# Optimization experiments

Hardware: AMD Instinct MI355X
Metric: run time of the kernel (lower is better)

Reference implementation:

```python
import jax, jax.numpy as jnp
import numpy as np
import math

B, S, HID = 1, 2048, 2048
H, QLR, KVLR = 16, 1536, 512
NOPE, ROPE, VD = 128, 64, 128
QKD = NOPE + ROPE


def rmsnorm(x, w, eps=1e-6):
    v = jnp.mean(x * x, axis=-1, keepdims=True)
    return w * (x * jax.lax.rsqrt(v + eps))


def rope_tables(seq_len, dim):
    inv_freq = 1.0 / (10000.0 ** (jnp.arange(0, dim, 2, dtype=jnp.float32) / dim))
    t = jnp.arange(seq_len, dtype=jnp.float32)[:, None]
    freqs = t * inv_freq[None, :]
    freqs = jnp.concatenate([freqs, freqs], axis=-1)  # [S, dim]
    return jnp.cos(freqs), jnp.sin(freqs)


def rotate_half(x):
    x1, x2 = jnp.split(x, 2, axis=-1)
    return jnp.concatenate([-x2, x1], axis=-1)


def setup_inputs() -> dict:
    key = jax.random.key(0)
    ks = jax.random.split(key, 8)
    s = 0.02
    return {
        'x': jax.random.normal(ks[0], (B, S, HID), jnp.float32),
        'wq_a_w': jax.random.normal(ks[1], (QLR, HID), jnp.float32) * s,
        'wq_a_b': jnp.zeros((QLR,), jnp.float32),
        'q_norm_w': jnp.ones((QLR,), jnp.float32),
        'wq_b_w': jax.random.normal(ks[2], (H * QKD, QLR), jnp.float32) * s,
        'wq_b_b': jnp.zeros((H * QKD,), jnp.float32),
        'wkv_a_w': jax.random.normal(ks[3], (KVLR + ROPE, HID), jnp.float32) * s,
        'wkv_a_b': jnp.zeros((KVLR + ROPE,), jnp.float32),
        'kv_norm_w': jnp.ones((KVLR,), jnp.float32),
        'wkv_b_w': jax.random.normal(ks[4], (H * (NOPE + VD), KVLR), jnp.float32) * s,
        'wo_w': jax.random.normal(ks[5], (HID, H * VD), jnp.float32) * s,
        'wo_b': jnp.zeros((HID,), jnp.float32),
    }


def reference(x, wq_a_w, wq_a_b, q_norm_w, wq_b_w, wq_b_b, wkv_a_w, wkv_a_b,
              kv_norm_w, wkv_b_w, wo_w, wo_b):
    bs, seq_len, _ = x.shape
    # low-rank q projection
    q = x @ wq_a_w.T + wq_a_b            # [B,S,QLR]
    q = rmsnorm(q, q_norm_w)
    q = q @ wq_b_w.T + wq_b_b            # [B,S,H*QKD]
    q = q.reshape(bs, seq_len, H, QKD)
    q_nope, q_pe = q[..., :NOPE], q[..., NOPE:]

    # latent kv + rope key
    kv_full = x @ wkv_a_w.T + wkv_a_b    # [B,S,KVLR+ROPE]
    kv, k_pe = kv_full[..., :KVLR], kv_full[..., KVLR:]

    cos, sin = rope_tables(seq_len, ROPE)        # [S,ROPE]
    cos4 = cos[None, :, None, :]
    sin4 = sin[None, :, None, :]
    q_pe = q_pe * cos4 + rotate_half(q_pe) * sin4          # [B,S,H,ROPE]
    k_pe = k_pe * cos[None] + rotate_half(k_pe) * sin[None]  # [B,S,ROPE]

    # absorbed kv projection
    wkv_b = wkv_b_w.reshape(H, NOPE + VD, KVLR)
    q_nope = jnp.einsum('bshd,hdc->bshc', q_nope, wkv_b[:, :NOPE])  # [B,S,H,KVLR]
    kv = rmsnorm(kv, kv_norm_w)                                     # [B,T,KVLR]

    scores = (jnp.einsum('bshc,btc->bsht', q_nope, kv)
              + jnp.einsum('bshr,btr->bsht', q_pe, k_pe)) / math.sqrt(QKD)
    # causal mask: position t > s masked
    s_idx = jnp.arange(seq_len)
    mask = jnp.where(s_idx[None, :, None, None] >= s_idx[None, None, None, :],
                     0.0, -jnp.inf)  # [1,S,1,T]
    scores = jax.nn.softmax(scores + mask, axis=-1)

    out = jnp.einsum('bsht,btc->bshc', scores, kv)            # [B,S,H,KVLR]
    out = jnp.einsum('bshc,hdc->bshd', out, wkv_b[:, NOPE:])  # [B,S,H,VD]
    out = out.reshape(bs, seq_len, H * VD)
    return out @ wo_w.T + wo_b
```

## Files before the change

### kernel.cpp

```cpp
#include <hip/hip_runtime.h>
#include <hip/hip_bf16.h>
#include <stdint.h>


using bf16 = __hip_bfloat16;
typedef __bf16 bf16x8 __attribute__((ext_vector_type(8)));
typedef __bf16 bf16x4 __attribute__((ext_vector_type(4)));
typedef float f32x4 __attribute__((ext_vector_type(4)));

#define S_LEN 2048
#define NHEAD 16

static __device__ __forceinline__ void gload16(const void* g, void* l) {
  __builtin_amdgcn_global_load_lds(
      (const __attribute__((address_space(1))) unsigned int*)g,
      (__attribute__((address_space(3))) unsigned int*)l, 16, 0, 0);
}

__global__ void cvt_all(const float* __restrict__ x, const float* __restrict__ wqa_s,
                        const float* __restrict__ wqb_s, const float* __restrict__ wkva_s,
                        const float* __restrict__ wkvb_s, const float* __restrict__ wo_s,
                        bf16* __restrict__ xb, bf16* __restrict__ wqa,
                        bf16* __restrict__ wqb, bf16* __restrict__ wkva,
                        bf16* __restrict__ wkvb, bf16* __restrict__ wob) {
  const size_t n0 = 1048576;
  const size_t n1 = n0 + 786432;
  const size_t n2 = n1 + 1179648;
  const size_t n3 = n2 + 327680;
  const size_t n4 = n3 + 524288;
  const size_t n5 = n4 + 1048576;
  auto cvt4 = [](const float4 v, bf16* d) {
    bf16x4 o;
    o[0] = (__bf16)__float2bfloat16(v.x);
    o[1] = (__bf16)__float2bfloat16(v.y);
    o[2] = (__bf16)__float2bfloat16(v.z);
    o[3] = (__bf16)__float2bfloat16(v.w);
    *(bf16x4*)d = o;
  };
  for (size_t i = (size_t)blockIdx.x * blockDim.x + threadIdx.x; i < n5;
       i += (size_t)gridDim.x * blockDim.x) {
    if (i < n0) {
      cvt4(*(const float4*)(x + i * 4), xb + i * 4);
    } else if (i < n1) {
      size_t j = i - n0;
      cvt4(*(const float4*)(wqa_s + j * 4), wqa + j * 4);
    } else if (i < n2) {
      size_t j = i - n1;
      cvt4(*(const float4*)(wqb_s + j * 4), wqb + j * 4);
    } else if (i < n3) {
      size_t j = i - n2;
      size_t e = j * 4;
      int r = (int)(e / 2048), c = (int)(e % 2048);
      float4 v = (r < 576) ? *(const float4*)(wkva_s + (size_t)r * 2048 + c)
                           : make_float4(0.f, 0.f, 0.f, 0.f);
      cvt4(v, wkva + e);
    } else if (i < n4) {
      size_t j = i - n3;
      cvt4(*(const float4*)(wkvb_s + j * 4), wkvb + j * 4);
    } else {
      size_t j = i - n4;
      cvt4(*(const float4*)(wo_s + j * 4), wob + j * 4);
    }
  }
}

__global__ void rmsnorm_bf16(const bf16* __restrict__ in, const float* __restrict__ w,
                             bf16* __restrict__ out, int cols) {
  const int r = blockIdx.x, tid = threadIdx.x;
  const bf16* row = in + (size_t)r * cols;
  float ss = 0.f;
  for (int c = tid; c < cols; c += 256) {
    float v = __bfloat162float(row[c]);
    ss += v * v;
  }
  for (int m = 32; m >= 1; m >>= 1) ss += __shfl_xor(ss, m, 64);
  __shared__ float red[4];
  if ((tid & 63) == 0) red[tid >> 6] = ss;
  __syncthreads();
  ss = red[0] + red[1] + red[2] + red[3];
  float inv = rsqrtf(ss / (float)cols + 1e-6f);
  for (int c = tid; c < cols; c += 256)
    out[(size_t)r * cols + c] = __float2bfloat16(__bfloat162float(row[c]) * inv * w[c]);
}

__global__ void kv_post(const float* __restrict__ kvf, const float* __restrict__ kvw,
                        bf16* __restrict__ kvn, bf16* __restrict__ Kh) {
  const int t = blockIdx.x, tid = threadIdx.x;
  const float* row = kvf + (size_t)t * 640;
  float ss = 0.f;
  for (int c = tid; c < 512; c += 256) { float v = row[c]; ss += v * v; }
  for (int m = 32; m >= 1; m >>= 1) ss += __shfl_xor(ss, m, 64);
  __shared__ float red[4];
  if ((tid & 63) == 0) red[tid >> 6] = ss;
  __syncthreads();
  ss = red[0] + red[1] + red[2] + red[3];
  float inv = rsqrtf(ss * (1.0f / 512.0f) + 1e-6f);
  for (int c = tid; c < 512; c += 256)
    kvn[(size_t)t * 512 + c] = __float2bfloat16(row[c] * inv * kvw[c]);
  if (tid < 32) {
    const int j = tid;
    float freq = expf(-(float)j * (1.0f / 32.0f) * 9.210340371976184f);
    float ang = (float)t * freq;
    float cs = cosf(ang), sn = sinf(ang);
    float x1 = row[512 + j];
    float x2 = row[512 + j + 32];
    bf16 o1 = __float2bfloat16(x1 * cs - x2 * sn);
    bf16 o2 = __float2bfloat16(x2 * cs + x1 * sn);
#pragma unroll
    for (int h = 0; h < 16; ++h) {
      bf16* kr = Kh + ((size_t)h * S_LEN + t) * 192 + 128;
      kr[j] = o1;
      kr[j + 32] = o2;
    }
  }
}

__global__ void q_rope(bf16* __restrict__ qv) {
  const int s = blockIdx.x, tid = threadIdx.x;
  for (int it = tid; it < 512; it += 256) {
    const int h = it >> 5, j = it & 31;
    float freq = expf(-(float)j * (1.0f / 32.0f) * 9.210340371976184f);
    float ang = (float)s * freq;
    float cs = cosf(ang), sn = sinf(ang);
    bf16* base = qv + (size_t)s * 3072 + h * 192 + 128;
    float x1 = __bfloat162float(base[j]);
    float x2 = __bfloat162float(base[j + 32]);
    base[j] = __float2bfloat16(x1 * cs - x2 * sn);
    base[j + 32] = __float2bfloat16(x2 * cs + x1 * sn);
  }
}

__global__ __launch_bounds__(256, 3)
void attn_flash(const bf16* __restrict__ qv, const bf16* __restrict__ Kh,
                const bf16* __restrict__ V2T, bf16* __restrict__ oabs) {
  const int lin = (int)blockIdx.x + 32 * (int)blockIdx.y;
  const int l2 = (lin & 7) * 64 + (lin >> 3);
  const int h = l2 >> 5;
  const int qb = 31 - (l2 & 31);
  const int tid = threadIdx.x, w = tid >> 6, lane = tid & 63;
  const int lo = lane & 15, hi = lane >> 4;
  __shared__ bf16 Kn[2][32 * 128];
  __shared__ bf16 Kr[2][32 * 64];
  __shared__ bf16 Vt[2][128 * 32];
  __shared__ bf16 Pl[4][16 * 40];
  const int q0 = qb * 64 + w * 16;
  const int q = q0 + lo;

  bf16x8 Qf[6];
  {
    const bf16* qp = qv + (size_t)(q0 + lo) * 3072 + h * 192 + hi * 8;
#pragma unroll
    for (int ks = 0; ks < 6; ++ks) Qf[ks] = *(const bf16x8*)(qp + ks * 32);
  }
  f32x4 o[8];
#pragma unroll
  for (int cg = 0; cg < 8; ++cg) o[cg] = (f32x4){0.f, 0.f, 0.f, 0.f};
  float mrow = -3e38f, lrow = 0.f;

  const bf16* khh = Kh + (size_t)h * S_LEN * 192;
  const bf16* vth = V2T + (size_t)h * 128 * S_LEN;

  auto stage = [&](int tt, int b) {
    const int t0s = tt * 32;
#pragma unroll
    for (int i = 0; i < 2; ++i) {
      const int c = w * 2 + i;
      const int row = c * 4 + (lane >> 4);
      gload16(khh + (size_t)(t0s + row) * 192 + (((lane & 15) ^ (row & 7)) << 3),
              &Kn[b][c * 512]);
    }
#pragma unroll
    for (int i = 0; i < 2; ++i) {
      const int c = w * 2 + i;
      const int row = c * 16 + (lane >> 2);
      gload16(vth + (size_t)row * S_LEN + t0s + ((lane & 3) << 3),
              &Vt[b][c * 512]);
    }
    {
      const int row = w * 8 + (lane >> 3);
      gload16(khh + (size_t)(t0s + row) * 192 + 128 + ((((lane & 7) ^ (row & 7))) << 3),
              &Kr[b][w * 512]);
    }
  };

  const int ntile = 2 * qb + 2;
  stage(0, 0);
  for (int t = 0; t < ntile; ++t) {
    __syncthreads();
    const int b = t & 1;
    if (t + 1 < ntile) stage(t + 1, b ^ 1);
    const int t0 = t * 32;

    f32x4 sc[2];
    sc[0] = (f32x4){0.f, 0.f, 0.f, 0.f};
    sc[1] = (f32x4){0.f, 0.f, 0.f, 0.f};
#pragma unroll
    for (int ks = 0; ks < 4; ++ks)
#pragma unroll
      for (int f = 0; f < 2; ++f) {
        const int row = f * 16 + lo;
        bf16x8 kf = *(const bf16x8*)&Kn[b][row * 128 + (((ks << 2) + hi) ^ (lo & 7)) * 8];
        sc[f] = __builtin_amdgcn_mfma_f32_16x16x32_bf16(kf, Qf[ks], sc[f], 0, 0, 0);
      }
#pragma unroll
    for (int kk2 = 0; kk2 < 2; ++kk2)
#pragma unroll
      for (int f = 0; f < 2; ++f) {
        const int row = f * 16 + lo;
        bf16x8 kf = *(const bf16x8*)&Kr[b][row * 64 + (((kk2 << 2) + hi) ^ (lo & 7)) * 8];
        sc[f] = __builtin_amdgcn_mfma_f32_16x16x32_bf16(kf, Qf[4 + kk2], sc[f], 0, 0, 0);
      }

    const bool diag = (t0 + 31 > q0);
    float rmax = -3e38f;
#pragma unroll
    for (int f = 0; f < 2; ++f)
#pragma unroll
      for (int j = 0; j < 4; ++j) {
        float v = sc[f][j] * 0.0721687836487032f;
        if (diag && (t0 + f * 16 + hi * 4 + j > q)) v = -3e38f;
        sc[f][j] = v;
        rmax = fmaxf(rmax, v);
      }
    rmax = fmaxf(rmax, __shfl_xor(rmax, 16, 64));
    rmax = fmaxf(rmax, __shfl_xor(rmax, 32, 64));

    const float mn = fmaxf(mrow, rmax);
    const float fsc = __expf(mrow - mn);
    mrow = mn;

    float rsum = 0.f;
    bf16* prow = &Pl[w][lo * 40];
#pragma unroll
    for (int f = 0; f < 2; ++f) {
      float pj[4];
#pragma unroll
      for (int j = 0; j < 4; ++j) {
        pj[j] = __expf(sc[f][j] - mn);
        rsum += pj[j];
      }
#pragma unroll
      for (int i2 = 0; i2 < 2; ++i2) {
        uint32_t lo16 = (uint32_t)__bfloat16_as_ushort(__float2bfloat16(pj[i2 * 2]));
        uint32_t hi16 = (uint32_t)__bfloat16_as_ushort(__float2bfloat16(pj[i2 * 2 + 1]));
        *(uint32_t*)(prow + f * 16 + hi * 4 + i2 * 2) = lo16 | (hi16 << 16);
      }
    }
    rsum += __shfl_xor(rsum, 16, 64);
    rsum += __shfl_xor(rsum, 32, 64);
    lrow = lrow * fsc + rsum;

    float fscO[4];
#pragma unroll
    for (int j = 0; j < 4; ++j) fscO[j] = __shfl(fsc, hi * 4 + j, 64);
#pragma unroll
    for (int cg = 0; cg < 8; ++cg)
#pragma unroll
      for (int j = 0; j < 4; ++j) o[cg][j] *= fscO[j];

    bf16x8 pa = *(const bf16x8*)&Pl[w][lo * 40 + hi * 8];
#pragma unroll
    for (int cg = 0; cg < 8; ++cg) {
      bf16x8 vf = *(const bf16x8*)&Vt[b][(cg * 16 + lo) * 32 + hi * 8];
      o[cg] = __builtin_amdgcn_mfma_f32_16x16x32_bf16(pa, vf, o[cg], 0, 0, 0);
    }
  }

  const float linv = 1.0f / lrow;
  float linvO[4];
#pragma unroll
  for (int j = 0; j < 4; ++j) linvO[j] = __shfl(linv, hi * 4 + j, 64);
  bf16* ob = oabs + (size_t)q0 * 2048 + h * 128;
#pragma unroll
  for (int j = 0; j < 4; ++j)
#pragma unroll
    for (int cg = 0; cg < 8; ++cg)
      ob[(size_t)(hi * 4 + j) * 2048 + cg * 16 + lo] =
          __float2bfloat16(o[cg][j] * linvO[j]);
}

template <bool BIAS, bool BF16OUT, int BM>
__global__ __launch_bounds__(256)
void gemm_bt(const bf16* __restrict__ A, const bf16* __restrict__ B,
             const float* __restrict__ bias, void* __restrict__ Cv,
             int lda, int ldb, int ldc, int K, int Nreal,
             long long bA, long long bB, long long bC, int mode) {
  int bx, byi, bz;
  {
    const int gx = gridDim.x, gy = gridDim.y;
    const int nwg = gx * gy * (int)gridDim.z;
    const int lin = (int)blockIdx.x + gx * ((int)blockIdx.y + gy * (int)blockIdx.z);
    const int cpx = nwg >> 3;
    const int l2 = (lin & 7) * cpx + (lin >> 3);
    bx = l2 % gx;
    byi = (l2 / gx) % gy;
    bz = l2 / (gx * gy);
    if (mode) byi = (bz & 1) ? byi : gy - 1 - byi;
  }
  const size_t m0 = (size_t)byi * BM, n0 = (size_t)bx * 128;
  if (mode == 1 && (int)n0 >= (int)m0 + BM) return;
  const int Keff = (mode == 2) ? ((K < (int)m0 + BM) ? K : (int)m0 + BM) : K;

  constexpr int ACH = BM / 8;
  constexpr int PER = (ACH + 16) / 4;
  constexpr int NFR = (BM == 64) ? 2 : 4;
  __shared__ bf16 As[2][BM * 64];
  __shared__ bf16 Bs[2][8192];
  const int tid = threadIdx.x;
  const int wave = tid >> 6, lane = tid & 63;
  const int lo = lane & 15, hi = lane >> 4;
  const int rowbase = (BM == 64) ? 0 : ((wave >> 1) * 64);
  const int colbase = (BM == 64) ? (wave * 32) : ((wave & 1) * 64);
  A += (size_t)bz * (size_t)bA;
  B += (size_t)bz * (size_t)bB;
  const int srow = lane >> 3;
  const int scol = (((lane & 7) ^ srow) * 8);
  const int rsw = lo & 7;

  auto stage = [&](int k0, int buf) {
#pragma unroll
    for (int i = 0; i < PER; ++i) {
      const int blk = wave * PER + i;
      if (blk < ACH) {
        const int row = blk * 8 + srow;
        gload16(A + (m0 + row) * (size_t)lda + k0 + scol, &As[buf][blk * 512]);
      } else {
        const int j = blk - ACH;
        const int row = j * 8 + srow;
        gload16(B + (n0 + row) * (size_t)ldb + k0 + scol, &Bs[buf][j * 512]);
      }
    }
  };

  f32x4 acc[4][NFR] = {};
  stage(0, 0);
  int cur = 0;
  for (int k0 = 0; k0 < Keff; k0 += 64) {
    __syncthreads();
    if (k0 + 64 < Keff) stage(k0 + 64, cur ^ 1);
#pragma unroll
    for (int kk = 0; kk < 2; ++kk) {
      const int ch = (((kk << 2) + hi) ^ rsw) << 3;
      bf16x8 af[4], bfr[NFR];
#pragma unroll
      for (int m = 0; m < 4; ++m)
        af[m] = *(const bf16x8*)&As[cur][(rowbase + m * 16 + lo) * 64 + ch];
#pragma unroll
      for (int n = 0; n < NFR; ++n)
        bfr[n] = *(const bf16x8*)&Bs[cur][(colbase + n * 16 + lo) * 64 + ch];
#pragma unroll
      for (int m = 0; m < 4; ++m)
#pragma unroll
        for (int n = 0; n < NFR; ++n)
          acc[m][n] = __builtin_amdgcn_mfma_f32_16x16x32_bf16(af[m], bfr[n], acc[m][n], 0, 0, 0);
    }
    cur ^= 1;
  }
  float* Cf = (float*)Cv;
  bf16* Cb = (bf16*)Cv;
  const size_t cbase = (size_t)bz * (size_t)bC;
#pragma unroll
  for (int m = 0; m < 4; ++m) {
    const size_t row = m0 + rowbase + m * 16 + hi * 4;
#pragma unroll
    for (int n = 0; n < NFR; ++n) {
      const int col = (int)n0 + colbase + n * 16 + lo;
      if (col < Nreal) {
        const float bv = BIAS ? bias[col] : 0.0f;
#pragma unroll
        for (int j = 0; j < 4; ++j) {
          const float v = acc[m][n][j] + bv;
          const size_t off = cbase + (row + j) * (size_t)ldc + col;
          if (BF16OUT) Cb[off] = __float2bfloat16(v);
          else         Cf[off] = v;
        }
      }
    }
  }
}

extern "C" void kernel_launch(void* const* d_in, const int* in_sizes, int n_in,
                              void* d_out, int out_size, void* d_ws, size_t ws_size,
                              hipStream_t stream) {
  const float* x       = (const float*)d_in[0];
  const float* wq_a_w  = (const float*)d_in[1];
  const float* wq_a_b  = (const float*)d_in[2];
  const float* q_norm  = (const float*)d_in[3];
  const float* wq_b_w  = (const float*)d_in[4];
  const float* wq_b_b  = (const float*)d_in[5];
  const float* wkv_a_w = (const float*)d_in[6];
  const float* wkv_a_b = (const float*)d_in[7];
  const float* kv_norm = (const float*)d_in[8];
  const float* wkv_b_w = (const float*)d_in[9];
  const float* wo_w    = (const float*)d_in[10];
  const float* wo_bias = (const float*)d_in[11];
  float* out = (float*)d_out;

  char* base = (char*)d_ws;
  bf16*  xb   = (bf16*)(base + 0);
  bf16*  wqa  = (bf16*)(base + 8388608);
  bf16*  wqb  = (bf16*)(base + 14680064);
  bf16*  wkva = (bf16*)(base + 24117248);
  bf16*  wkvb = (bf16*)(base + 26738688);
  bf16*  qa   = (bf16*)(base + 30932992);
  bf16*  qn   = (bf16*)(base + 37224448);
  float* kvf  = (float*)(base + 43515904);
  bf16*  kvn  = (bf16*)(base + 48758784);
  char* q = base + 134217728;
  bf16* qv   = (bf16*)(q);             q += 12582912;
  bf16* Kh   = (bf16*)(q);             q += 12582912;
  bf16* V2T  = (bf16*)(q);             q += 8388608;
  bf16* wob  = (bf16*)(q);             q += 8388608;
  bf16* oabs = (bf16*)(q);             q += 8388608;

  cvt_all<<<dim3(2048), 256, 0, stream>>>(x, wq_a_w, wq_b_w, wkv_a_w, wkv_b_w, wo_w,
                                          xb, wqa, wqb, wkva, wkvb, wob);

  gemm_bt<true, true, 64><<<dim3(12, 32, 1), 256, 0, stream>>>(
      xb, wqa, wq_a_b, qa, 2048, 2048, 1536, 2048, 1536, 0, 0, 0, 0);
  rmsnorm_bf16<<<2048, 256, 0, stream>>>(qa, q_norm, qn, 1536);
  gemm_bt<true, true, 128><<<dim3(24, 16, 1), 256, 0, stream>>>(
      qn, wqb, wq_b_b, qv, 1536, 1536, 3072, 1536, 3072, 0, 0, 0, 0);
  q_rope<<<2048, 256, 0, stream>>>(qv);
  gemm_bt<true, false, 64><<<dim3(5, 32, 1), 256, 0, stream>>>(
      xb, wkva, wkv_a_b, kvf, 2048, 2048, 640, 2048, 576, 0, 0, 0, 0);
  kv_post<<<2048, 256, 0, stream>>>(kvf, kv_norm, kvn, Kh);
  gemm_bt<false, true, 64><<<dim3(1, 32, 16), 256, 0, stream>>>(
      kvn, wkvb, nullptr, Kh, 512, 512, 192, 512, 128,
      0, 256ll * 512, 2048ll * 192, 0);
  gemm_bt<false, true, 64><<<dim3(16, 2, 16), 256, 0, stream>>>(
      wkvb + 128ull * 512, kvn, nullptr, V2T, 512, 512, 2048, 512, 2048,
      256ll * 512, 0, 128ll * 2048, 0);

  attn_flash<<<dim3(32, 16), 256, 0, stream>>>(qv, Kh, V2T, oabs);

  gemm_bt<true, false, 64><<<dim3(16, 32, 1), 256, 0, stream>>>(
      oabs, wob, wo_bias, out, 2048, 2048, 2048, 2048, 2048, 0, 0, 0, 0);
}
```

Before: 258.7 us.

## Use 64-key tiles in flash attention, load rope keys from global, skip rescales

The attention kernel now processes 64 keys per iteration instead of 32, which halves the number of tile iterations and barriers. V tiles get an XOR swizzle, and the rope-key part is loaded straight from global memory into registers instead of being staged in LDS. Rescaling of the output accumulator is skipped when no row's running max changes. The larger LDS footprint and more registers drop the occupancy target from 3 to 2 blocks per SM, and the direct global rope loads may add latency.

```diff
diff --git a/kernel.cpp b/kernel.cpp
--- a/kernel.cpp
+++ b/kernel.cpp
@@ -130,7 +130,7 @@
   }
 }
 
-__global__ __launch_bounds__(256, 3)
+__global__ __launch_bounds__(256, 2)
 void attn_flash(const bf16* __restrict__ qv, const bf16* __restrict__ Kh,
                 const bf16* __restrict__ V2T, bf16* __restrict__ oabs) {
   const int lin = (int)blockIdx.x + 32 * (int)blockIdx.y;
@@ -139,10 +139,9 @@
   const int qb = 31 - (l2 & 31);
   const int tid = threadIdx.x, w = tid >> 6, lane = tid & 63;
   const int lo = lane & 15, hi = lane >> 4;
-  __shared__ bf16 Kn[2][32 * 128];
-  __shared__ bf16 Kr[2][32 * 64];
-  __shared__ bf16 Vt[2][128 * 32];
-  __shared__ bf16 Pl[4][16 * 40];
+  __shared__ bf16 Kn[2][64 * 128];
+  __shared__ bf16 Vt[2][128 * 64];
+  __shared__ bf16 Pl[4][16 * 72];
   const int q0 = qb * 64 + w * 16;
   const int q = q0 + lo;
 
@@ -161,60 +160,61 @@
   const bf16* vth = V2T + (size_t)h * 128 * S_LEN;
 
   auto stage = [&](int tt, int b) {
-    const int t0s = tt * 32;
-#pragma unroll
-    for (int i = 0; i < 2; ++i) {
-      const int c = w * 2 + i;
+    const int t0s = tt * 64;
+#pragma unroll
+    for (int i = 0; i < 4; ++i) {
+      const int c = w * 4 + i;
       const int row = c * 4 + (lane >> 4);
       gload16(khh + (size_t)(t0s + row) * 192 + (((lane & 15) ^ (row & 7)) << 3),
               &Kn[b][c * 512]);
     }
 #pragma unroll
-    for (int i = 0; i < 2; ++i) {
-      const int c = w * 2 + i;
-      const int row = c * 16 + (lane >> 2);
-      gload16(vth + (size_t)row * S_LEN + t0s + ((lane & 3) << 3),
+    for (int i = 0; i < 4; ++i) {
+      const int c = w * 4 + i;
+      const int row = c * 8 + (lane >> 3);
+      gload16(vth + (size_t)row * S_LEN + t0s + (((lane & 7) ^ (row & 7)) << 3),
               &Vt[b][c * 512]);
     }
-    {
-      const int row = w * 8 + (lane >> 3);
-      gload16(khh + (size_t)(t0s + row) * 192 + 128 + ((((lane & 7) ^ (row & 7))) << 3),
-              &Kr[b][w * 512]);
-    }
   };
 
-  const int ntile = 2 * qb + 2;
+  const int ntile = qb + 1;
   stage(0, 0);
   for (int t = 0; t < ntile; ++t) {
     __syncthreads();
     const int b = t & 1;
+    const int t0 = t * 64;
+
+    bf16x8 rk[2][4];
+#pragma unroll
+    for (int ks2 = 0; ks2 < 2; ++ks2)
+#pragma unroll
+      for (int f = 0; f < 4; ++f)
+        rk[ks2][f] = *(const bf16x8*)(khh + (size_t)(t0 + f * 16 + lo) * 192 + 128 +
+                                      ks2 * 32 + hi * 8);
+
     if (t + 1 < ntile) stage(t + 1, b ^ 1);
-    const int t0 = t * 32;
-
-    f32x4 sc[2];
-    sc[0] = (f32x4){0.f, 0.f, 0.f, 0.f};
-    sc[1] = (f32x4){0.f, 0.f, 0.f, 0.f};
+
+    f32x4 sc[4];
+#pragma unroll
+    for (int f = 0; f < 4; ++f) sc[f] = (f32x4){0.f, 0.f, 0.f, 0.f};
 #pragma unroll
     for (int ks = 0; ks < 4; ++ks)
 #pragma unroll
-      for (int f = 0; f < 2; ++f) {
+      for (int f = 0; f < 4; ++f) {
         const int row = f * 16 + lo;
-        bf16x8 kf = *(const bf16x8*)&Kn[b][row * 128 + (((ks << 2) + hi) ^ (lo & 7)) * 8];
+        bf16x8 kf = *(const bf16x8*)&Kn[b][row * 128 + ((((ks << 2) + hi) ^ (row & 7)) << 3)];
         sc[f] = __builtin_amdgcn_mfma_f32_16x16x32_bf16(kf, Qf[ks], sc[f], 0, 0, 0);
       }
 #pragma unroll
-    for (int kk2 = 0; kk2 < 2; ++kk2)
-#pragma unroll
-      for (int f = 0; f < 2; ++f) {
-        const int row = f * 16 + lo;
-        bf16x8 kf = *(const bf16x8*)&Kr[b][row * 64 + (((kk2 << 2) + hi) ^ (lo & 7)) * 8];
-        sc[f] = __builtin_amdgcn_mfma_f32_16x16x32_bf16(kf, Qf[4 + kk2], sc[f], 0, 0, 0);
-      }
-
-    const bool diag = (t0 + 31 > q0);
+    for (int ks2 = 0; ks2 < 2; ++ks2)
+#pragma unroll
+      for (int f = 0; f < 4; ++f)
+        sc[f] = __builtin_amdgcn_mfma_f32_16x16x32_bf16(rk[ks2][f], Qf[4 + ks2], sc[f], 0, 0, 0);
+
+    const bool diag = (t == qb);
     float rmax = -3e38f;
 #pragma unroll
-    for (int f = 0; f < 2; ++f)
+    for (int f = 0; f < 4; ++f)
 #pragma unroll
       for (int j = 0; j < 4; ++j) {
         float v = sc[f][j] * 0.0721687836487032f;
@@ -225,18 +225,28 @@
     rmax = fmaxf(rmax, __shfl_xor(rmax, 16, 64));
     rmax = fmaxf(rmax, __shfl_xor(rmax, 32, 64));
 
-    const float mn = fmaxf(mrow, rmax);
-    const float fsc = __expf(mrow - mn);
-    mrow = mn;
+    if (!__all(rmax <= mrow)) {
+      const float mn = fmaxf(mrow, rmax);
+      const float fsc = __expf(mrow - mn);
+      mrow = mn;
+      lrow *= fsc;
+      float fscO[4];
+#pragma unroll
+      for (int j = 0; j < 4; ++j) fscO[j] = __shfl(fsc, hi * 4 + j, 64);
+#pragma unroll
+      for (int cg = 0; cg < 8; ++cg)
+#pragma unroll
+        for (int j = 0; j < 4; ++j) o[cg][j] *= fscO[j];
+    }
 
     float rsum = 0.f;
-    bf16* prow = &Pl[w][lo * 40];
-#pragma unroll
-    for (int f = 0; f < 2; ++f) {
+    bf16* prow = &Pl[w][lo * 72];
+#pragma unroll
+    for (int f = 0; f < 4; ++f) {
       float pj[4];
 #pragma unroll
       for (int j = 0; j < 4; ++j) {
-        pj[j] = __expf(sc[f][j] - mn);
+        pj[j] = __expf(sc[f][j] - mrow);
         rsum += pj[j];
       }
 #pragma unroll
@@ -248,21 +258,17 @@
     }
     rsum += __shfl_xor(rsum, 16, 64);
     rsum += __shfl_xor(rsum, 32, 64);
-    lrow = lrow * fsc + rsum;
-
-    float fscO[4];
-#pragma unroll
-    for (int j = 0; j < 4; ++j) fscO[j] = __shfl(fsc, hi * 4 + j, 64);
-#pragma unroll
-    for (int cg = 0; cg < 8; ++cg)
-#pragma unroll
-      for (int j = 0; j < 4; ++j) o[cg][j] *= fscO[j];
-
-    bf16x8 pa = *(const bf16x8*)&Pl[w][lo * 40 + hi * 8];
-#pragma unroll
-    for (int cg = 0; cg < 8; ++cg) {
-      bf16x8 vf = *(const bf16x8*)&Vt[b][(cg * 16 + lo) * 32 + hi * 8];
-      o[cg] = __builtin_amdgcn_mfma_f32_16x16x32_bf16(pa, vf, o[cg], 0, 0, 0);
+    lrow += rsum;
+
+#pragma unroll
+    for (int tk = 0; tk < 2; ++tk) {
+      bf16x8 pa = *(const bf16x8*)&Pl[w][lo * 72 + tk * 32 + hi * 8];
+#pragma unroll
+      for (int cg = 0; cg < 8; ++cg) {
+        const int vrow = cg * 16 + lo;
+        bf16x8 vf = *(const bf16x8*)&Vt[b][vrow * 64 + ((((tk << 2) + hi) ^ (vrow & 7)) << 3)];
+        o[cg] = __builtin_amdgcn_mfma_f32_16x16x32_bf16(pa, vf, o[cg], 0, 0, 0);
+      }
     }
   }
 
```

New measurement: 251.3 us. 1.03x faster.
